# Performance work log

Measured on AMD Instinct MI355X. Metric: run time of the kernel, lower is better.

Reference implementation:

```python
import jax, jax.numpy as jnp
import numpy as np

DIM = 1024
MLP_DIM = 4096
EPS = 1e-5


def layer_norm(x, gamma, beta):
    mean = jnp.mean(x, axis=-1, keepdims=True)
    var = jnp.mean(jnp.square(x - mean), axis=-1, keepdims=True)  # unbiased=False
    return gamma * (x - mean) / jnp.sqrt(var + EPS) + beta


def setup_inputs() -> dict:
    key = jax.random.key(0)
    ks = jax.random.split(key, 12)
    s = 0.02
    return {
        "x": jax.random.normal(ks[0], (4, 2048, DIM), dtype=jnp.float32),
        "gamma1": jnp.ones((DIM,), jnp.float32),
        "beta1": jnp.zeros((DIM,), jnp.float32),
        "gamma2": jnp.ones((DIM,), jnp.float32),
        "beta2": jnp.zeros((DIM,), jnp.float32),
        "Wq": jax.random.normal(ks[1], (DIM, DIM), jnp.float32) * s,
        "bq": jnp.zeros((DIM,), jnp.float32),
        "Wk": jax.random.normal(ks[2], (DIM, DIM), jnp.float32) * s,
        "bk": jnp.zeros((DIM,), jnp.float32),
        "Wv": jax.random.normal(ks[3], (DIM, DIM), jnp.float32) * s,
        "bv": jnp.zeros((DIM,), jnp.float32),
        "W1": jax.random.normal(ks[4], (DIM, MLP_DIM), jnp.float32) * s,
        "b1": jnp.zeros((MLP_DIM,), jnp.float32),
        "W2": jax.random.normal(ks[5], (MLP_DIM, DIM), jnp.float32) * s,
        "b2": jnp.zeros((DIM,), jnp.float32),
    }


def reference(x, gamma1, beta1, gamma2, beta2, Wq, bq, Wk, bk, Wv, bv, W1, b1, W2, b2):
    # Pre-LN attention sub-block (single-head manual attention over full dim)
    residual = x
    h = layer_norm(x, gamma1, beta1)
    q = h @ Wq + bq  # [B,S,D]
    k = h @ Wk + bk
    v = h @ Wv + bv
    scale = 1.0 / jnp.sqrt(jnp.asarray(q.shape[-1], q.dtype))
    scores = jnp.einsum("bsd,btd->bst", q, k) * scale  # [B,S,S]
    attn = jax.nn.softmax(scores, axis=-1)
    x = jnp.einsum("bst,btd->bsd", attn, v) + residual
    # Pre-LN MLP sub-block
    residual = x
    h = layer_norm(x, gamma2, beta2)
    h = jax.nn.gelu(h @ W1 + b1, approximate=False)  # torch F.gelu exact
    x = h @ W2 + b2 + residual
    return x
```

## Files before the change

### kernel.cpp

```cpp
#include <hip/hip_runtime.h>
#include <hip/hip_bf16.h>
#include <math.h>

typedef __bf16 bf16x8 __attribute__((ext_vector_type(8)));
typedef float  f32x4  __attribute__((ext_vector_type(4)));
typedef __hip_bfloat16 bf16;

#define DIM  1024
#define MLPD 4096
#define NB   4
#define SEQ  2048
#define ROWS (NB * SEQ)

__device__ __forceinline__ void gload_lds16(const void* g, void* l) {
  __builtin_amdgcn_global_load_lds(
      (__attribute__((address_space(1))) void*)(g),
      (__attribute__((address_space(3))) void*)(l), 16, 0, 0);
}

__device__ __forceinline__ void bar() {
  asm volatile("" ::: "memory");
  __builtin_amdgcn_s_barrier();
  asm volatile("" ::: "memory");
}

template <int N>
__device__ __forceinline__ void vmw() {
  asm volatile("s_waitcnt vmcnt(%0)" ::"n"(N) : "memory");
}

__device__ __forceinline__ bf16 to_bf16(float v) { return __float2bfloat16(v); }
__device__ __forceinline__ bf16 to_bf16(bf16 v)  { return v; }

__device__ __forceinline__ float gelu_exact_fast(float v) {
  const float x  = v * 0.70710678118654752f;
  const float ax = fabsf(x);
  const float t  = __builtin_amdgcn_rcpf(1.0f + 0.3275911f * ax);
  const float p  = t * (0.254829592f +
                   t * (-0.284496736f +
                   t * (1.421413741f +
                   t * (-1.453152027f + t * 1.061405429f))));
  float erf = 1.0f - p * __expf(-x * x);
  erf = copysignf(erf, x);
  return 0.5f * v * (1.0f + erf);
}

template <int EPI>
__global__ __launch_bounds__(256, 4) void gemm128(
    const bf16* __restrict__ A,  long aBatch, int lda,
    const bf16* __restrict__ Bt, long bBatch, int ldb,
    void* __restrict__ Cout,     long cBatch, int ldc,
    const float* __restrict__ bias,
    const float* __restrict__ resid, long rBatch, int ldr,
    int K, float scale)
{
  __shared__ char smem[2][16384];

  const int gx = gridDim.x, gy = gridDim.y;
  const int n = gx * gy * gridDim.z;
  const int f = blockIdx.x + gx * (blockIdx.y + gy * blockIdx.z);
  const int o = (f & 7) * (n >> 3) + (f >> 3);
  const int sx = gx >> 3;
  int st = o >> 6;
  const int w = o & 63;
  const int spz = sx * (gy >> 3);
  const int bz = st / spz; st -= bz * spz;
  const int sty = st / sx, stx = st - sty * sx;
  const int by = sty * 8 + (w >> 3), bx = stx * 8 + (w & 7);

  const long rowBase = (long)by * 128;
  const long colBase = (long)bx * 128;
  const long ldaB = (long)lda * 2, ldbB = (long)ldb * 2;
  const char* Ag = (const char*)(A + bz * aBatch + rowBase * lda);
  const char* Bg = (const char*)(Bt + bz * bBatch + colBase * ldb);

  const int tid  = threadIdx.x;
  const int lane = tid & 63;
  const int wave = tid >> 6;
  const int wm = wave >> 1, wn = wave & 1;
  const int fr = lane & 15, fq = lane >> 4;

  const int fh = fr >> 1;
  const int sA = (((fr & 1) << 2) | fq) ^ fh;
  const int laneRd = fh * 128 + sA * 16;
  const int abase = wm * 4096 + laneRd;
  const int bbase = 8192 + wn * 4096 + laneRd;

  const int t0   = wave * 128 + lane;
  const int r2   = t0 >> 3;
  const int u0   = (t0 & 7) ^ (r2 & 7);
  const int row0 = r2 * 2 + (u0 >> 2);
  const int kc0  = u0 & 3;
  const char* aSrc0 = Ag + (long)row0 * ldaB + kc0 * 16;
  const char* aSrc1 = aSrc0 + 16 * ldaB;
  const char* bSrc0 = Bg + (long)row0 * ldbB + kc0 * 16;
  const char* bSrc1 = bSrc0 + 16 * ldbB;
  const int doff = wave * 2048 + lane * 16;

  const int NT = K >> 5;
  f32x4 acc[4][4] = {};

#define STAGE(WB)                                                              \
  do {                                                                         \
    gload_lds16(aSrc0, &smem[WB][doff]);                                       \
    gload_lds16(aSrc1, &smem[WB][doff + 1024]);                                \
    gload_lds16(bSrc0, &smem[WB][8192 + doff]);                                \
    gload_lds16(bSrc1, &smem[WB][8192 + doff + 1024]);                         \
    aSrc0 += 64; aSrc1 += 64; bSrc0 += 64; bSrc1 += 64;                        \
  } while (0)

#define READMM(RB)                                                             \
  do {                                                                         \
    const char* _r = &smem[RB][0];                                             \
    bf16x8 av[4], bv[4];                                                       \
    _Pragma("unroll") for (int m = 0; m < 4; ++m)                              \
      av[m] = *(const bf16x8*)(_r + abase + m * 1024);                         \
    _Pragma("unroll") for (int nn = 0; nn < 4; ++nn)                           \
      bv[nn] = *(const bf16x8*)(_r + bbase + nn * 1024);                       \
    __builtin_amdgcn_s_setprio(1);                                             \
    _Pragma("unroll") for (int m = 0; m < 4; ++m)                              \
      _Pragma("unroll") for (int nn = 0; nn < 4; ++nn)                         \
        acc[m][nn] = __builtin_amdgcn_mfma_f32_16x16x32_bf16(                  \
            av[m], bv[nn], acc[m][nn], 0, 0, 0);                               \
    __builtin_amdgcn_s_setprio(0);                                             \
  } while (0)

  STAGE(0); STAGE(1);
  vmw<4>(); bar();

  for (int t = 0; t < NT; t += 2) {
    READMM(0);
    vmw<0>(); bar();
    if (t + 2 < NT) STAGE(0);
    READMM(1);
    bar();
    if (t + 3 < NT) STAGE(1);
    vmw<4>(); bar();
  }

#undef STAGE
#undef READMM

#pragma unroll
  for (int m = 0; m < 4; ++m) {
#pragma unroll
    for (int nn = 0; nn < 4; ++nn) {
      const long col = colBase + wn * 64 + nn * 16 + fr;
#pragma unroll
      for (int e = 0; e < 4; ++e) {
        const long r = rowBase + wm * 64 + m * 16 + fq * 4 + e;
        float v = acc[m][nn][e];
        if constexpr (EPI == 0) {
          v += bias[col];
          ((bf16*)Cout)[bz * cBatch + r * ldc + col] = __float2bfloat16(v);
        } else if constexpr (EPI == 2) {
          v += resid[bz * rBatch + r * ldr + col];
          ((float*)Cout)[bz * cBatch + r * ldc + col] = v;
        } else if constexpr (EPI == 3) {
          v += bias[col];
          ((bf16*)Cout)[bz * cBatch + r * ldc + col] =
              __float2bfloat16(gelu_exact_fast(v));
        } else if constexpr (EPI == 4) {
          v += bias[col] + resid[r * (long)ldr + col];
          ((float*)Cout)[bz * cBatch + r * ldc + col] = v;
        } else {
          ((bf16*)Cout)[bz * cBatch + r * ldc + col] = __float2bfloat16(v * scale);
        }
      }
    }
  }
}

__global__ __launch_bounds__(256) void ln_kernel(
    const float* __restrict__ x, const float* __restrict__ gamma,
    const float* __restrict__ beta, bf16* __restrict__ out)
{
  const long row = blockIdx.x;
  const float4 v = ((const float4*)(x + row * DIM))[threadIdx.x];
  float s  = v.x + v.y + v.z + v.w;
  float ss = v.x * v.x + v.y * v.y + v.z * v.z + v.w * v.w;
  const int lane = threadIdx.x & 63, wave = threadIdx.x >> 6;
#pragma unroll
  for (int o = 32; o; o >>= 1) { s += __shfl_xor(s, o); ss += __shfl_xor(ss, o); }
  __shared__ float rs[4], rss[4];
  if (lane == 0) { rs[wave] = s; rss[wave] = ss; }
  __syncthreads();
  s  = rs[0] + rs[1] + rs[2] + rs[3];
  ss = rss[0] + rss[1] + rss[2] + rss[3];
  const float mean = s * (1.0f / DIM);
  const float var  = ss * (1.0f / DIM) - mean * mean;
  const float rstd = rsqrtf(var + 1e-5f);
  const float4 g = ((const float4*)gamma)[threadIdx.x];
  const float4 b = ((const float4*)beta)[threadIdx.x];
  union { bf16 h[4]; uint2 u; } pk;
  pk.h[0] = __float2bfloat16(g.x * (v.x - mean) * rstd + b.x);
  pk.h[1] = __float2bfloat16(g.y * (v.y - mean) * rstd + b.y);
  pk.h[2] = __float2bfloat16(g.z * (v.z - mean) * rstd + b.z);
  pk.h[3] = __float2bfloat16(g.w * (v.w - mean) * rstd + b.w);
  ((uint2*)(out + row * DIM))[threadIdx.x] = pk.u;
}

__global__ __launch_bounds__(256) void softmax_kernel(bf16* __restrict__ scores)
{
  const long row = blockIdx.x;
  bf16* rp = scores + row * (long)SEQ;
  union { bf16 h[8]; uint4 u; } in;
  in.u = ((const uint4*)rp)[threadIdx.x];
  float f[8];
#pragma unroll
  for (int j = 0; j < 8; ++j) f[j] = __bfloat162float(in.h[j]);
  const int lane = threadIdx.x & 63, wave = threadIdx.x >> 6;
  float mx = f[0];
#pragma unroll
  for (int j = 1; j < 8; ++j) mx = fmaxf(mx, f[j]);
#pragma unroll
  for (int o = 32; o; o >>= 1) mx = fmaxf(mx, __shfl_xor(mx, o));
  __shared__ float rm[4], rsum[4];
  if (lane == 0) rm[wave] = mx;
  __syncthreads();
  mx = fmaxf(fmaxf(rm[0], rm[1]), fmaxf(rm[2], rm[3]));
  float sum = 0.0f;
#pragma unroll
  for (int j = 0; j < 8; ++j) { f[j] = expf(f[j] - mx); sum += f[j]; }
#pragma unroll
  for (int o = 32; o; o >>= 1) sum += __shfl_xor(sum, o);
  if (lane == 0) rsum[wave] = sum;
  __syncthreads();
  sum = rsum[0] + rsum[1] + rsum[2] + rsum[3];
  const float inv = 1.0f / sum;
  union { bf16 h[8]; uint4 u; } pk;
#pragma unroll
  for (int j = 0; j < 8; ++j) pk.h[j] = __float2bfloat16(f[j] * inv);
  ((uint4*)rp)[threadIdx.x] = pk.u;
}

template <typename TI>
__global__ __launch_bounds__(256) void transpose_bf16_kernel(
    const TI* __restrict__ in, bf16* __restrict__ out,
    int ldIn, int ldOut, long inBatch, long outBatch)
{
  __shared__ bf16 tile[32][33];
  const long zin  = (long)blockIdx.z * inBatch;
  const long zout = (long)blockIdx.z * outBatch;
  const int c0 = blockIdx.x * 32, r0 = blockIdx.y * 32;
  const int tx = threadIdx.x & 31, ty = threadIdx.x >> 5;
#pragma unroll
  for (int i = 0; i < 32; i += 8)
    tile[ty + i][tx] = to_bf16(in[zin + (long)(r0 + ty + i) * ldIn + c0 + tx]);
  __syncthreads();
#pragma unroll
  for (int i = 0; i < 32; i += 8)
    out[zout + (long)(c0 + ty + i) * ldOut + r0 + tx] = tile[tx][ty + i];
}

__global__ __launch_bounds__(256) void concat3_kernel(
    const float* __restrict__ a, const float* __restrict__ b,
    const float* __restrict__ c, float* __restrict__ o)
{
  const int i = blockIdx.x * 256 + threadIdx.x;
  if (i < DIM) { o[i] = a[i]; o[DIM + i] = b[i]; o[2 * DIM + i] = c[i]; }
}

extern "C" void kernel_launch(void* const* d_in, const int* in_sizes, int n_in,
                              void* d_out, int out_size, void* d_ws, size_t ws_size,
                              hipStream_t stream) {
  const float* x   = (const float*)d_in[0];
  const float* g1  = (const float*)d_in[1];
  const float* be1 = (const float*)d_in[2];
  const float* g2  = (const float*)d_in[3];
  const float* be2 = (const float*)d_in[4];
  const float* Wq  = (const float*)d_in[5];
  const float* bq  = (const float*)d_in[6];
  const float* Wk  = (const float*)d_in[7];
  const float* bk  = (const float*)d_in[8];
  const float* Wv  = (const float*)d_in[9];
  const float* bv  = (const float*)d_in[10];
  const float* W1  = (const float*)d_in[11];
  const float* b1  = (const float*)d_in[12];
  const float* W2  = (const float*)d_in[13];
  const float* b2  = (const float*)d_in[14];
  float* out = (float*)d_out;

  char* ws = (char*)d_ws;
  bf16* WqkvT = (bf16*)(ws + 0);
  bf16* W1T   = (bf16*)(ws + (6l << 20));
  bf16* W2T   = (bf16*)(ws + (14l << 20));
  float* bqkv = (float*)(ws + (22l << 20));
  bf16* h     = (bf16*)(ws + (23l << 20));
  bf16* qkv   = (bf16*)(ws + (39l << 20));
  bf16* vT    = (bf16*)(ws + (87l << 20));
  bf16* sc    = (bf16*)(ws + (103l << 20));
  bf16* g_act = (bf16*)sc;

  const dim3 blk(256);

  concat3_kernel<<<4, blk, 0, stream>>>(bq, bk, bv, bqkv);
  transpose_bf16_kernel<float><<<dim3(32, 32, 1), blk, 0, stream>>>(
      Wq, WqkvT, DIM, DIM, 0, 0);
  transpose_bf16_kernel<float><<<dim3(32, 32, 1), blk, 0, stream>>>(
      Wk, WqkvT + (long)DIM * DIM, DIM, DIM, 0, 0);
  transpose_bf16_kernel<float><<<dim3(32, 32, 1), blk, 0, stream>>>(
      Wv, WqkvT + 2l * DIM * DIM, DIM, DIM, 0, 0);
  transpose_bf16_kernel<float><<<dim3(128, 32, 1), blk, 0, stream>>>(
      W1, W1T, MLPD, DIM, 0, 0);
  transpose_bf16_kernel<float><<<dim3(32, 128, 1), blk, 0, stream>>>(
      W2, W2T, DIM, MLPD, 0, 0);

  ln_kernel<<<ROWS, blk, 0, stream>>>(x, g1, be1, h);

  gemm128<0><<<dim3(24, 64, 1), blk, 0, stream>>>(
      h, 0, DIM, WqkvT, 0, DIM, qkv, 0, 3 * DIM,
      bqkv, nullptr, 0, 0, DIM, 1.0f);

  transpose_bf16_kernel<bf16><<<dim3(32, 64, NB), blk, 0, stream>>>(
      qkv + 2 * DIM, vT, 3 * DIM, SEQ, (long)SEQ * 3 * DIM, (long)DIM * SEQ);

  gemm128<5><<<dim3(16, 16, NB), blk, 0, stream>>>(
      qkv, (long)SEQ * 3 * DIM, 3 * DIM, qkv + DIM, (long)SEQ * 3 * DIM, 3 * DIM,
      sc, (long)SEQ * SEQ, SEQ, nullptr, nullptr, 0, 0, DIM, 0.03125f);

  softmax_kernel<<<ROWS, blk, 0, stream>>>(sc);

  gemm128<2><<<dim3(8, 16, NB), blk, 0, stream>>>(
      sc, (long)SEQ * SEQ, SEQ, vT, (long)DIM * SEQ, SEQ,
      out, (long)SEQ * DIM, DIM, nullptr, x, (long)SEQ * DIM, DIM, SEQ, 1.0f);

  ln_kernel<<<ROWS, blk, 0, stream>>>(out, g2, be2, h);

  gemm128<3><<<dim3(32, 64, 1), blk, 0, stream>>>(
      h, 0, DIM, W1T, 0, DIM, g_act, 0, MLPD, b1, nullptr, 0, 0, DIM, 1.0f);

  gemm128<4><<<dim3(8, 64, 1), blk, 0, stream>>>(
      g_act, 0, MLPD, W2T, 0, MLPD, out, 0, DIM, b2, out, 0, DIM, MLPD, 1.0f);
}
```

Baseline: 382.0 us.

## Give each wave private LDS tiles to remove block barriers in GEMM

Each of the four waves now stages its own A and B sub-tiles into a private double-buffered LDS region and synchronizes only with its own waitcnt, eliminating workgroup barriers. This removes barrier stalls between waves, but doubles global/L2 load traffic because A and B slices are fetched redundantly by waves sharing rows or columns. LDS use grows to 64KB per block and launch bounds drop to two blocks per CU, lowering occupancy.

After: 489.4 us. 1.28x slower.

```diff
diff --git a/kernel.cpp b/kernel.cpp
--- a/kernel.cpp
+++ b/kernel.cpp
@@ -18,15 +18,13 @@
       (__attribute__((address_space(3))) void*)(l), 16, 0, 0);
 }
 
-__device__ __forceinline__ void bar() {
-  asm volatile("" ::: "memory");
-  __builtin_amdgcn_s_barrier();
-  asm volatile("" ::: "memory");
-}
-
 template <int N>
 __device__ __forceinline__ void vmw() {
   asm volatile("s_waitcnt vmcnt(%0)" ::"n"(N) : "memory");
+}
+
+__device__ __forceinline__ void lgkm0() {
+  asm volatile("s_waitcnt lgkmcnt(0)" ::: "memory");
 }
 
 __device__ __forceinline__ bf16 to_bf16(float v) { return __float2bfloat16(v); }
@@ -46,7 +44,7 @@
 }
 
 template <int EPI>
-__global__ __launch_bounds__(256, 4) void gemm128(
+__global__ __launch_bounds__(256, 2) void gemm128(
     const bf16* __restrict__ A,  long aBatch, int lda,
     const bf16* __restrict__ Bt, long bBatch, int ldb,
     void* __restrict__ Cout,     long cBatch, int ldc,
@@ -54,7 +52,7 @@
     const float* __restrict__ resid, long rBatch, int ldr,
     int K, float scale)
 {
-  __shared__ char smem[2][16384];
+  __shared__ char smem[4][16384];
 
   const int gx = gridDim.x, gy = gridDim.y;
   const int n = gx * gy * gridDim.z;
@@ -81,42 +79,46 @@
   const int fr = lane & 15, fq = lane >> 4;
 
   const int fh = fr >> 1;
-  const int sA = (((fr & 1) << 2) | fq) ^ fh;
+  const int sA = (((fr & 1) << 2) | fq) ^ (fh & 7);
   const int laneRd = fh * 128 + sA * 16;
-  const int abase = wm * 4096 + laneRd;
-  const int bbase = 8192 + wn * 4096 + laneRd;
-
-  const int t0   = wave * 128 + lane;
-  const int r2   = t0 >> 3;
-  const int u0   = (t0 & 7) ^ (r2 & 7);
-  const int row0 = r2 * 2 + (u0 >> 2);
-  const int kc0  = u0 & 3;
-  const char* aSrc0 = Ag + (long)row0 * ldaB + kc0 * 16;
-  const char* aSrc1 = aSrc0 + 16 * ldaB;
-  const char* bSrc0 = Bg + (long)row0 * ldbB + kc0 * 16;
-  const char* bSrc1 = bSrc0 + 16 * ldbB;
-  const int doff = wave * 2048 + lane * 16;
+  char* wbase = &smem[wave][0];
+
+  int offA[4], offB[4];
+#pragma unroll
+  for (int li = 0; li < 4; ++li) {
+    const int tt = li * 64 + lane;
+    const int rr = tt >> 3;
+    const int uu = (tt & 7) ^ (rr & 7);
+    const int srow = rr * 2 + (uu >> 2);
+    const int skc  = (uu & 3) * 16;
+    offA[li] = (wm * 64 + srow) * (int)ldaB + skc;
+    offB[li] = (wn * 64 + srow) * (int)ldbB + skc;
+  }
+  const int dBase = lane * 16;
 
   const int NT = K >> 5;
   f32x4 acc[4][4] = {};
 
-#define STAGE(WB)                                                              \
+#define STAGE(P, JB)                                                           \
   do {                                                                         \
-    gload_lds16(aSrc0, &smem[WB][doff]);                                       \
-    gload_lds16(aSrc1, &smem[WB][doff + 1024]);                                \
-    gload_lds16(bSrc0, &smem[WB][8192 + doff]);                                \
-    gload_lds16(bSrc1, &smem[WB][8192 + doff + 1024]);                         \
-    aSrc0 += 64; aSrc1 += 64; bSrc0 += 64; bSrc1 += 64;                        \
+    char* _d = wbase + (P) * 8192 + dBase;                                     \
+    _Pragma("unroll") for (int li = 0; li < 4; ++li) {                         \
+      gload_lds16(Ag + (JB) + offA[li], _d + li * 1024);                       \
+      gload_lds16(Bg + (JB) + offB[li], _d + 4096 + li * 1024);                \
+    }                                                                          \
   } while (0)
 
-#define READMM(RB)                                                             \
+#define TILE(T, P)                                                             \
   do {                                                                         \
-    const char* _r = &smem[RB][0];                                             \
+    if ((T) == NT - 1) vmw<0>(); else vmw<8>();                                \
+    const char* _r = wbase + (P) * 8192 + laneRd;                              \
     bf16x8 av[4], bv[4];                                                       \
     _Pragma("unroll") for (int m = 0; m < 4; ++m)                              \
-      av[m] = *(const bf16x8*)(_r + abase + m * 1024);                         \
+      av[m] = *(const bf16x8*)(_r + m * 1024);                                 \
     _Pragma("unroll") for (int nn = 0; nn < 4; ++nn)                           \
-      bv[nn] = *(const bf16x8*)(_r + bbase + nn * 1024);                       \
+      bv[nn] = *(const bf16x8*)(_r + 4096 + nn * 1024);                        \
+    lgkm0();                                                                   \
+    if ((T) + 2 < NT) STAGE(P, ((T) + 2) * 64);                                \
     __builtin_amdgcn_s_setprio(1);                                             \
     _Pragma("unroll") for (int m = 0; m < 4; ++m)                              \
       _Pragma("unroll") for (int nn = 0; nn < 4; ++nn)                         \
@@ -125,21 +127,16 @@
     __builtin_amdgcn_s_setprio(0);                                             \
   } while (0)
 
-  STAGE(0); STAGE(1);
-  vmw<4>(); bar();
+  STAGE(0, 0);
+  STAGE(1, 64);
 
   for (int t = 0; t < NT; t += 2) {
-    READMM(0);
-    vmw<0>(); bar();
-    if (t + 2 < NT) STAGE(0);
-    READMM(1);
-    bar();
-    if (t + 3 < NT) STAGE(1);
-    vmw<4>(); bar();
+    TILE(t, 0);
+    TILE(t + 1, 1);
   }
 
 #undef STAGE
-#undef READMM
+#undef TILE
 
 #pragma unroll
   for (int m = 0; m < 4; ++m) {
```

## Add 256x256-tile GEMM with 8 waves for QKV, scores and MLP1

Applied to the files above, without the earlier changes.

Adds a new gemm256 kernel that uses 512-thread blocks, 256x256 output tiles, 128 KB of dynamic LDS, a swizzled layout and a finer-grained interleaved prefetch schedule. It is used for the QKV, score and W1 GEMMs. The goal is more data reuse per block and fewer global loads per FLOP. The old gemm128, still used for the PV and W2 GEMMs, loses its double-buffered prefetch and now loads then waits each iteration, which exposes load latency there. The dead epilogue branches are also removed from gemm128.

New measurement: 372.8 us. -2.4%, faster.

```diff
diff --git a/kernel.cpp b/kernel.cpp
--- a/kernel.cpp
+++ b/kernel.cpp
@@ -43,6 +43,176 @@
   float erf = 1.0f - p * __expf(-x * x);
   erf = copysignf(erf, x);
   return 0.5f * v * (1.0f + erf);
+}
+
+__device__ __forceinline__ void epi_store(
+    int EPI_, void* Cout, long idx, float v, long col,
+    const float* bias, const float* resid, long ridx, float scale);
+
+template <int EPI>
+__global__ __launch_bounds__(512, 2) void gemm256(
+    const bf16* __restrict__ A,  long aBatch, int lda,
+    const bf16* __restrict__ Bt, long bBatch, int ldb,
+    void* __restrict__ Cout,     long cBatch, int ldc,
+    const float* __restrict__ bias, int K, float scale)
+{
+  extern __shared__ char smem[];
+
+  const int gx = gridDim.x, gy = gridDim.y;
+  int flat = blockIdx.x + gx * (blockIdx.y + gy * blockIdx.z);
+  const int nwg = gx * gy * gridDim.z;
+  flat = (flat & 7) * (nwg >> 3) + (flat >> 3);
+  const int bx = flat % gx;
+  const int t2 = flat / gx;
+  const int by = t2 % gy;
+  const int bz = t2 / gy;
+
+  const long rowBase = (long)by * 256;
+  const long colBase = (long)bx * 256;
+  const long ldaB = (long)lda * 2, ldbB = (long)ldb * 2;
+  const char* Ag = (const char*)(A + bz * aBatch + rowBase * lda);
+  const char* Bg = (const char*)(Bt + bz * bBatch + colBase * ldb);
+
+  const int tid  = threadIdx.x;
+  const int lane = tid & 63;
+  const int wave = tid >> 6;
+  const int wm = wave >> 2, wn = wave & 3;
+  const int fr = lane & 15, fq = lane >> 4;
+  const int fh2 = fr >> 1;
+  const int sA = (((fr & 1) << 2) | fq) ^ fh2;
+  const int rdCom = fh2 * 128 + sA * 16;
+
+  long offA[2], offB[2];
+#pragma unroll
+  for (int li = 0; li < 2; ++li) {
+    const int d = li * 512 + tid;
+    {
+      const int wms = d >> 9, kks = (d >> 8) & 1, w = d & 255;
+      const int pr = w >> 3, s = w & 7, u = s ^ (pr & 7);
+      offA[li] = (long)(wms * 128 + pr * 2 + (u >> 2)) * ldaB +
+                 kks * 64 + (u & 3) * 16;
+    }
+    {
+      const int wns = d >> 8, kkb = (d >> 7) & 1, w = d & 127;
+      const int pr = w >> 3, s = w & 7, u = s ^ (pr & 7);
+      offB[li] = (long)(wns * 64 + pr * 2 + (u >> 2)) * ldbB +
+                 kkb * 64 + (u & 3) * 16;
+    }
+  }
+  const int dstOff = tid * 16;
+  const long aHalf = ldaB << 6;
+  const long bHalf = ldbB << 5;
+
+  const int NT = K >> 6;
+
+  bf16x8 a[4][2], b[2][2][2];
+  f32x4 acc[8][4] = {};
+
+#define STG_A(J, mh)                                                           \
+  do {                                                                         \
+    char* _d = smem + (((J) & 1) << 16) + (mh) * 16384 + dstOff;               \
+    const char* _s = Ag + (J) * 128 + (mh) * aHalf;                            \
+    gload_lds16(_s + offA[0], _d);                                             \
+    gload_lds16(_s + offA[1], _d + 8192);                                      \
+  } while (0)
+
+#define STG_B(J, nh)                                                           \
+  do {                                                                         \
+    char* _d = smem + (((J) & 1) << 16) + 32768 + (nh) * 16384 + dstOff;       \
+    const char* _s = Bg + (J) * 128 + (nh) * bHalf;                            \
+    gload_lds16(_s + offB[0], _d);                                             \
+    gload_lds16(_s + offB[1], _d + 8192);                                      \
+  } while (0)
+
+#define LDA(mh, J)                                                             \
+  do {                                                                         \
+    const char* _b = smem + (((J) & 1) << 16) + (mh) * 16384 + wm * 8192 +     \
+                     rdCom;                                                    \
+    _Pragma("unroll") for (int m = 0; m < 4; ++m)                              \
+      _Pragma("unroll") for (int kk = 0; kk < 2; ++kk)                         \
+        a[m][kk] = *(const bf16x8*)(_b + kk * 4096 + m * 1024);                \
+  } while (0)
+
+#define LDB(nh, J)                                                             \
+  do {                                                                         \
+    const char* _b = smem + (((J) & 1) << 16) + 32768 + (nh) * 16384 +         \
+                     wn * 4096 + rdCom;                                        \
+    _Pragma("unroll") for (int n = 0; n < 2; ++n)                              \
+      _Pragma("unroll") for (int kk = 0; kk < 2; ++kk)                         \
+        b[nh][n][kk] = *(const bf16x8*)(_b + kk * 2048 + n * 1024);            \
+  } while (0)
+
+#define MM(mh, nh)                                                             \
+  do {                                                                         \
+    __builtin_amdgcn_s_setprio(1);                                             \
+    _Pragma("unroll") for (int m = 0; m < 4; ++m)                              \
+      _Pragma("unroll") for (int n = 0; n < 2; ++n)                            \
+        _Pragma("unroll") for (int kk = 0; kk < 2; ++kk)                       \
+          acc[(mh) * 4 + m][(nh) * 2 + n] =                                    \
+              __builtin_amdgcn_mfma_f32_16x16x32_bf16(                         \
+                  a[m][kk], b[nh][n][kk], acc[(mh) * 4 + m][(nh) * 2 + n],     \
+                  0, 0, 0);                                                    \
+    __builtin_amdgcn_s_setprio(0);                                             \
+  } while (0)
+
+#define LGKM0 asm volatile("s_waitcnt lgkmcnt(0)" ::: "memory")
+
+#define TILE(J, S1, S2, VN)                                                    \
+  do {                                                                         \
+    LDA(0, J); LDB(0, J);                                                      \
+    if (S1) STG_A((J) + 1, 1);                                                 \
+    bar(); LGKM0; MM(0, 0); bar();                                             \
+    LDB(1, J);                                                                 \
+    if (S2) STG_A((J) + 2, 0);                                                 \
+    bar(); LGKM0; MM(0, 1); bar();                                             \
+    LDA(1, J);                                                                 \
+    if (S2) STG_B((J) + 2, 0);                                                 \
+    bar(); LGKM0; MM(1, 1); bar();                                             \
+    if (S2) STG_B((J) + 2, 1);                                                 \
+    vmw<VN>(); bar(); MM(1, 0); bar();                                         \
+  } while (0)
+
+  STG_A(0, 0); STG_B(0, 0); STG_B(0, 1); STG_A(0, 1);
+  STG_A(1, 0); STG_B(1, 0); STG_B(1, 1);
+  vmw<6>(); bar();
+
+  for (int j = 0; j < NT - 2; ++j) TILE(j, true, true, 6);
+  TILE(NT - 2, true, false, 0);
+  TILE(NT - 1, false, false, 63);
+
+#undef STG_A
+#undef STG_B
+#undef LDA
+#undef LDB
+#undef MM
+#undef TILE
+
+#pragma unroll
+  for (int mh = 0; mh < 2; ++mh)
+#pragma unroll
+    for (int m = 0; m < 4; ++m)
+#pragma unroll
+      for (int nh = 0; nh < 2; ++nh)
+#pragma unroll
+        for (int n = 0; n < 2; ++n) {
+          const long col = colBase + wn * 64 + nh * 32 + n * 16 + fr;
+#pragma unroll
+          for (int e = 0; e < 4; ++e) {
+            const long r = rowBase + wm * 128 + mh * 64 + m * 16 + fq * 4 + e;
+            float v = acc[mh * 4 + m][nh * 2 + n][e];
+            if constexpr (EPI == 0) {
+              v += bias[col];
+              ((bf16*)Cout)[bz * cBatch + r * ldc + col] = __float2bfloat16(v);
+            } else if constexpr (EPI == 3) {
+              v += bias[col];
+              ((bf16*)Cout)[bz * cBatch + r * ldc + col] =
+                  __float2bfloat16(gelu_exact_fast(v));
+            } else {
+              ((bf16*)Cout)[bz * cBatch + r * ldc + col] =
+                  __float2bfloat16(v * scale);
+            }
+          }
+        }
 }
 
 template <int EPI>
@@ -125,17 +295,13 @@
     __builtin_amdgcn_s_setprio(0);                                             \
   } while (0)
 
-  STAGE(0); STAGE(1);
-  vmw<4>(); bar();
-
   for (int t = 0; t < NT; t += 2) {
+    STAGE(0);
+    STAGE(1);
+    vmw<0>(); bar();
     READMM(0);
-    vmw<0>(); bar();
-    if (t + 2 < NT) STAGE(0);
     READMM(1);
     bar();
-    if (t + 3 < NT) STAGE(1);
-    vmw<4>(); bar();
   }
 
 #undef STAGE
@@ -150,21 +316,12 @@
       for (int e = 0; e < 4; ++e) {
         const long r = rowBase + wm * 64 + m * 16 + fq * 4 + e;
         float v = acc[m][nn][e];
-        if constexpr (EPI == 0) {
-          v += bias[col];
-          ((bf16*)Cout)[bz * cBatch + r * ldc + col] = __float2bfloat16(v);
-        } else if constexpr (EPI == 2) {
+        if constexpr (EPI == 2) {
           v += resid[bz * rBatch + r * ldr + col];
           ((float*)Cout)[bz * cBatch + r * ldc + col] = v;
-        } else if constexpr (EPI == 3) {
-          v += bias[col];
-          ((bf16*)Cout)[bz * cBatch + r * ldc + col] =
-              __float2bfloat16(gelu_exact_fast(v));
-        } else if constexpr (EPI == 4) {
+        } else {
           v += bias[col] + resid[r * (long)ldr + col];
           ((float*)Cout)[bz * cBatch + r * ldc + col] = v;
-        } else {
-          ((bf16*)Cout)[bz * cBatch + r * ldc + col] = __float2bfloat16(v * scale);
         }
       }
     }
@@ -292,7 +449,15 @@
   bf16* sc    = (bf16*)(ws + (103l << 20));
   bf16* g_act = (bf16*)sc;
 
-  const dim3 blk(256);
+  const int SMEM = 131072;
+  hipFuncSetAttribute(reinterpret_cast<const void*>(&gemm256<0>),
+                      hipFuncAttributeMaxDynamicSharedMemorySize, SMEM);
+  hipFuncSetAttribute(reinterpret_cast<const void*>(&gemm256<3>),
+                      hipFuncAttributeMaxDynamicSharedMemorySize, SMEM);
+  hipFuncSetAttribute(reinterpret_cast<const void*>(&gemm256<5>),
+                      hipFuncAttributeMaxDynamicSharedMemorySize, SMEM);
+
+  const dim3 blk(256), gblk(512);
 
   concat3_kernel<<<4, blk, 0, stream>>>(bq, bk, bv, bqkv);
   transpose_bf16_kernel<float><<<dim3(32, 32, 1), blk, 0, stream>>>(
@@ -308,16 +473,15 @@
 
   ln_kernel<<<ROWS, blk, 0, stream>>>(x, g1, be1, h);
 
-  gemm128<0><<<dim3(24, 64, 1), blk, 0, stream>>>(
-      h, 0, DIM, WqkvT, 0, DIM, qkv, 0, 3 * DIM,
-      bqkv, nullptr, 0, 0, DIM, 1.0f);
+  gemm256<0><<<dim3(12, 32, 1), gblk, SMEM, stream>>>(
+      h, 0, DIM, WqkvT, 0, DIM, qkv, 0, 3 * DIM, bqkv, DIM, 1.0f);
 
   transpose_bf16_kernel<bf16><<<dim3(32, 64, NB), blk, 0, stream>>>(
       qkv + 2 * DIM, vT, 3 * DIM, SEQ, (long)SEQ * 3 * DIM, (long)DIM * SEQ);
 
-  gemm128<5><<<dim3(16, 16, NB), blk, 0, stream>>>(
-      qkv, (long)SEQ * 3 * DIM, 3 * DIM, qkv + DIM, (long)SEQ * 3 * DIM, 3 * DIM,
-      sc, (long)SEQ * SEQ, SEQ, nullptr, nullptr, 0, 0, DIM, 0.03125f);
+  gemm256<5><<<dim3(8, 8, NB), gblk, SMEM, stream>>>(
+      qkv, (long)SEQ * 3 * DIM, 3 * DIM, qkv + DIM, (long)SEQ * 3 * DIM,
+      3 * DIM, sc, (long)SEQ * SEQ, SEQ, nullptr, DIM, 0.03125f);
 
   softmax_kernel<<<ROWS, blk, 0, stream>>>(sc);
 
@@ -327,8 +491,8 @@
 
   ln_kernel<<<ROWS, blk, 0, stream>>>(out, g2, be2, h);
 
-  gemm128<3><<<dim3(32, 64, 1), blk, 0, stream>>>(
-      h, 0, DIM, W1T, 0, DIM, g_act, 0, MLPD, b1, nullptr, 0, 0, DIM, 1.0f);
+  gemm256<3><<<dim3(16, 32, 1), gblk, SMEM, stream>>>(
+      h, 0, DIM, W1T, 0, DIM, g_act, 0, MLPD, b1, DIM, 1.0f);
 
   gemm128<4><<<dim3(8, 64, 1), blk, 0, stream>>>(
       g_act, 0, MLPD, W2T, 0, MLPD, out, 0, DIM, b2, out, 0, DIM, MLPD, 1.0f);
```
